# Kernel optimization log

Hardware: AMD Instinct MI355X
Metric: run time of the kernel (lower is better)

## Reference

```python
import jax, jax.numpy as jnp
import numpy as np
from functools import partial

B, S, I, H, O, L = 32, 512, 1024, 1024, 1024, 2


def setup_inputs() -> dict:
    key = jax.random.key(0)
    ks = jax.random.split(key, 7)
    sc = 0.02  # keep gates out of saturation, like nn.Linear init scale
    return {
        "x": jax.random.normal(ks[0], (B, S, I), jnp.float32),
        "h0": jax.random.normal(ks[1], (B, L, H), jnp.float32) * sc,
        "Wx": jax.random.normal(ks[2], (L, 3 * H, I), jnp.float32) * sc,
        "bx": jax.random.normal(ks[3], (L, 3 * H), jnp.float32) * sc,
        "Wh": jax.random.normal(ks[4], (L, 3 * H, H), jnp.float32) * sc,
        "Why": jax.random.normal(ks[5], (O, H), jnp.float32) * sc,
        "bhy": jax.random.normal(ks[6], (O,), jnp.float32) * sc,
    }


def _gru_layer(xproj, h0, Whz, Whr, Whg):
    # xproj: [S, B, 3H] precomputed x-side projections; h0: [B, H]
    def step(h, xp):
        xz, xr, xg = jnp.split(xp, 3, axis=-1)
        z = jax.nn.sigmoid(xz + h @ Whz.T)
        r = jax.nn.sigmoid(xr + h @ Whr.T)
        # NOTE: original code uses sigmoid (not tanh) for the candidate g
        g = jax.nn.sigmoid(xg + (r * h) @ Whg.T)
        h = z * h + (1.0 - z) * g
        return h, h

    hT, ys = jax.lax.scan(step, h0, xproj)
    return hT, ys  # ys: [S, B, H]


def reference(x, h0, Wx, bx, Wh, Why, bhy):
    # x: [B,S,I], h0: [B,L,H]
    inp = x
    finals = []
    for l in range(L):
        # one big GEMM for all timesteps / all three gates on the x side
        xproj = jnp.einsum("bsi,gi->sbg", inp, Wx[l]) + bx[l]  # [S,B,3H]
        Whz, Whr, Whg = jnp.split(Wh[l], 3, axis=0)
        hT, ys = _gru_layer(xproj, h0[:, l, :], Whz, Whr, Whg)
        finals.append(hT)
        inp = jnp.transpose(ys, (1, 0, 2))  # [B,S,H]
    out = jnp.einsum("bsh,oh->bso", inp, Why) + bhy  # [B,S,O]
    hidden = jnp.stack(finals, axis=1)  # [B,L,H]
    return out, hidden
```

## Files before the change

kernel.cpp:

```cpp
#include <hip/hip_runtime.h>
#include <stdint.h>


typedef __bf16 bf16x8 __attribute__((ext_vector_type(8)));
typedef float f32x4 __attribute__((ext_vector_type(4)));
typedef unsigned short u16;
typedef unsigned int u32;
typedef u32 u32x2 __attribute__((ext_vector_type(2)));
typedef u32 u32x4 __attribute__((ext_vector_type(4)));

typedef __attribute__((address_space(1))) u32 as1_u32;
typedef __attribute__((address_space(3))) u32 as3_u32;

__device__ __forceinline__ u16 f2bf(float f) {
  union { float f; u32 u; } a; a.f = f;
  u32 u = a.u;
  u32 r = (u + 0x7fffu + ((u >> 16) & 1u)) >> 16;
  return (u16)r;
}
__device__ __forceinline__ float bf2f(u16 b) {
  union { u32 u; float f; } a; a.u = ((u32)b) << 16;
  return a.f;
}
__device__ __forceinline__ float sigmoidf_(float x) {
  return 1.0f / (1.0f + __expf(-x));
}
__device__ __forceinline__ bf16x8 as_bf(u32x4 q) {
  union { u32x4 q; bf16x8 v; } u; u.q = q; return u.v;
}

#define MFMA16(a, b, c) __builtin_amdgcn_mfma_f32_16x16x32_bf16((a), (b), (c), 0, 0, 0)

__device__ __forceinline__ void gll16(const void* g, void* l) {
  __builtin_amdgcn_global_load_lds((as1_u32*)g, (as3_u32*)l, 16, 0, 0);
}

__device__ __forceinline__ u32x4 ld_sc16(const void* p) {
  u32x4 r;
  asm volatile("global_load_dwordx4 %0, %1, off sc0 sc1" : "=v"(r) : "v"(p) : "memory");
  return r;
}
__device__ __forceinline__ u32x2 ld_sc8(const void* p) {
  u32x2 r;
  asm volatile("global_load_dwordx2 %0, %1, off sc0 sc1" : "=v"(r) : "v"(p) : "memory");
  return r;
}
__device__ __forceinline__ void st_sc2(void* p, u16 v) {
  u32 w = v;
  asm volatile("global_store_short %0, %1, off sc0 sc1" :: "v"(p), "v"(w) : "memory");
}
__device__ __forceinline__ void st_sc8(void* p, u32x2 v) {
  asm volatile("global_store_dwordx2 %0, %1, off sc0 sc1" :: "v"(p), "v"(v) : "memory");
}
__device__ __forceinline__ void st_sc16(void* p, u32x4 v) {
  asm volatile("global_store_dwordx4 %0, %1, off sc0 sc1" :: "v"(p), "v"(v) : "memory");
}
__device__ __forceinline__ void wait_vm0() {
  asm volatile("s_waitcnt vmcnt(0)" ::: "memory");
  __builtin_amdgcn_sched_barrier(0);
}
__device__ __forceinline__ int ldflag(const int* p) {
  int r;
  asm volatile("global_load_dword %0, %1, off sc0 sc1\n\ts_waitcnt vmcnt(0)"
               : "=v"(r) : "v"(p) : "memory");
  return r;
}
__device__ __forceinline__ void stflag(int* p, int v) {
  asm volatile("global_store_dword %0, %1, off sc0 sc1" :: "v"(p), "v"(v) : "memory");
}

__device__ __forceinline__ void signal_flag(int* flag, int val) {
  asm volatile("s_waitcnt vmcnt(0)" ::: "memory");
  __syncthreads();
  if (threadIdx.x == 0) stflag(flag, val);
}
__device__ __forceinline__ void wait_flags(int* flags, int nf, int target, int tid) {
  if (tid < 64) {
    for (;;) {
      int v = (tid < nf) ? ldflag(flags + tid * 32) : target;
      if (__all(v >= target)) break;
      __builtin_amdgcn_s_sleep(2);
    }
  }
  __syncthreads();
}
__device__ __forceinline__ void wait_flags2(int* f1, int n1, int t1,
                                            int* f2, int n2, int t2, int tid) {
  if (tid < 64) {
    const int* addr = nullptr;
    int tgt = 0, active = 0;
    if (tid < n1) { addr = f1 + tid * 32; tgt = t1; active = 1; }
    else if (tid < n1 + n2) { addr = f2 + (tid - n1) * 32; tgt = t2; active = 1; }
    for (;;) {
      int v = active ? ldflag(addr) : 0;
      int sat = (!active) || (v >= tgt);
      if (__all(sat)) break;
      __builtin_amdgcn_s_sleep(2);
    }
  }
  __syncthreads();
}

__device__ __forceinline__ void stage_issue16(const u16* g, u32x4* v, int tid) {
#pragma unroll
  for (int it = 0; it < 4; ++it) {
    int cc = tid + it * 512;
    int row = cc >> 7, sc = cc & 127;
    int gsc = sc ^ (row & 7);
    v[it] = ld_sc16((const char*)g + (size_t)(row * 128 + gsc) * 16);
  }
}
__device__ __forceinline__ void stage_write16(u16* lds, const u32x4* v, int tid) {
#pragma unroll
  for (int it = 0; it < 4; ++it) {
    int cc = tid + it * 512;
    *(u32x4*)((char*)lds + (size_t)cc * 16) = v[it];
  }
}
__device__ __forceinline__ u32x4 read_frag_sw(const u16* lds, int row, int kt, int hi4) {
  int cc = kt * 4 + hi4;
  int sc = cc ^ (row & 7);
  return *(const u32x4*)((const char*)lds + (size_t)row * 2048 + (size_t)sc * 16);
}

__device__ __forceinline__ void load_Bf(u32x4* Bf, const u16* W, int n_g, int hi4) {
  const u16* wrow = W + (size_t)n_g * 1024 + 8 * hi4;
#pragma unroll
  for (int kt = 0; kt < 32; ++kt) Bf[kt] = *(const u32x4*)(wrow + kt * 32);
}

__global__ __launch_bounds__(512, 1) void gru_pipe_kernel(
    const u16* __restrict__ xproj,
    const u16* __restrict__ Whb,
    const u16* __restrict__ Wx1,
    const float* __restrict__ bx,
    const float* __restrict__ h0in,
    u16* __restrict__ h0ring,
    u16* __restrict__ h1_bf,
    u16* __restrict__ rh0,
    u16* __restrict__ rh1,
    float* __restrict__ z0_t,
    float* __restrict__ z1_t,
    u16* __restrict__ xp1t,
    u16* __restrict__ ys1,
    float* __restrict__ hidden,
    int* __restrict__ bar)
{
  __shared__ u16 smem[16 * 1024];
  const int tid = (int)threadIdx.x;
  const int lane = tid & 63;
  const int wv = tid >> 6;
  const int wg = (int)blockIdx.x;
  const int col = lane & 15;
  const int hi4 = lane >> 4;

  int* A0 = bar;
  int* B0 = bar + 1024;
  int* A1 = bar + 1536;
  int* B1 = bar + 2560;
  int* X  = bar + 3072;

  if (wg < 16) {
    const int gw = wg * 8 + wv;
    const int n_g = gw * 16 + col;
    const bool is_z = (wg < 8);
    const int rc = n_g - 1024;
    u32x4 Bf[32];
    load_Bf(Bf, Whb, n_g, hi4);
    for (int s = 0; s < 512; ++s) {
#pragma unroll
      for (int g2 = 0; g2 < 2; ++g2) {
        float xpv[4];
        {
          const u16* xb = xproj + (size_t)s * (32 * 3072) + (size_t)(g2 * 16 + hi4 * 4) * 3072 + n_g;
#pragma unroll
          for (int j = 0; j < 4; ++j) xpv[j] = bf2f(xb[(size_t)j * 3072]);
        }
        wait_flags(B0 + g2 * 256, 8, s, tid);
        u32x4 v[4];
        stage_issue16(h0ring + g2 * 65536 + (size_t)((s - 1) & 3) * 16384, v, tid);
        wait_vm0();
        stage_write16(smem, v, tid);
        __syncthreads();
        f32x4 acc = {0.f, 0.f, 0.f, 0.f};
#pragma unroll
        for (int kt = 0; kt < 32; ++kt)
          acc = MFMA16(as_bf(read_frag_sw(smem, col, kt, hi4)), as_bf(Bf[kt]), acc);
        if (is_z) {
          union { float f[4]; u32x4 q; } q0;
#pragma unroll
          for (int j = 0; j < 4; ++j) q0.f[j] = sigmoidf_(xpv[j] + acc[j]);
          st_sc16(&z0_t[g2 * 16384 + n_g * 16 + hi4 * 4], q0.q);
        } else {
#pragma unroll
          for (int j = 0; j < 4; ++j) {
            int bl = hi4 * 4 + j;
            float rv = sigmoidf_(xpv[j] + acc[j]);
            u16 hraw = smem[bl * 1024 + ((((rc >> 3) ^ (bl & 7)) << 3) | (rc & 7))];
            st_sc2(&rh0[g2 * 16384 + bl * 1024 + rc], f2bf(rv * bf2f(hraw)));
          }
        }
        signal_flag(&A0[g2 * 512 + wg * 32], s + 1);
      }
    }
  } else if (wg < 24) {
    const int wgl = wg - 16;
    const int gw = 128 + wgl * 8 + wv;
    const int n_g = gw * 16 + col;
    const int gc = n_g - 2048;
    u32x4 Bf[32];
    load_Bf(Bf, Whb, n_g, hi4);
    float h_reg[2][4];
#pragma unroll
    for (int g2 = 0; g2 < 2; ++g2)
#pragma unroll
      for (int j = 0; j < 4; ++j)
        h_reg[g2][j] = h0in[(g2 * 16 + hi4 * 4 + j) * 2048 + gc];
    for (int s = 0; s < 512; ++s) {
#pragma unroll
      for (int g2 = 0; g2 < 2; ++g2) {
        float xpv[4];
        {
          const u16* xb = xproj + (size_t)s * (32 * 3072) + (size_t)(g2 * 16 + hi4 * 4) * 3072 + n_g;
#pragma unroll
          for (int j = 0; j < 4; ++j) xpv[j] = bf2f(xb[(size_t)j * 3072]);
        }
        wait_flags2(A0 + g2 * 512, 16, s + 1, X + g2 * 768, 24, s - 3, tid);
        u32x4 v[4];
        stage_issue16(rh0 + g2 * 16384, v, tid);
        u32x4 zq = ld_sc16(&z0_t[g2 * 16384 + gc * 16 + hi4 * 4]);
        wait_vm0();
        stage_write16(smem, v, tid);
        __syncthreads();
        f32x4 acc = {0.f, 0.f, 0.f, 0.f};
#pragma unroll
        for (int kt = 0; kt < 32; ++kt)
          acc = MFMA16(as_bf(read_frag_sw(smem, col, kt, hi4)), as_bf(Bf[kt]), acc);
        union { u32x4 q; float f[4]; } zz; zz.q = zq;
        u16* hslot = h0ring + g2 * 65536 + (size_t)(s & 3) * 16384;
#pragma unroll
        for (int j = 0; j < 4; ++j) {
          int bl = hi4 * 4 + j;
          float gv = sigmoidf_(xpv[j] + acc[j]);
          float hn = zz.f[j] * h_reg[g2][j] + (1.0f - zz.f[j]) * gv;
          h_reg[g2][j] = hn;
          st_sc2(&hslot[bl * 1024 + gc], f2bf(hn));
        }
        signal_flag(&B0[g2 * 256 + wgl * 32], s + 1);
        if (s == 511) {
#pragma unroll
          for (int j = 0; j < 4; ++j)
            hidden[(g2 * 16 + hi4 * 4 + j) * 2048 + gc] = h_reg[g2][j];
        }
      }
    }
  } else if (wg < 48) {
    const int wgx = wg - 24;
    const int gw = wgx * 8 + wv;
    const int n_g = gw * 16 + col;
    u32x4 Bf[32];
    load_Bf(Bf, Wx1, n_g, hi4);
    const float bias = bx[3072 + n_g];
    for (int t = 0; t < 512; ++t) {
#pragma unroll
      for (int g2 = 0; g2 < 2; ++g2) {
        wait_flags2(B0 + g2 * 256, 8, t + 1, B1 + g2 * 256, 8, t - 3, tid);
        u32x4 v[4];
        stage_issue16(h0ring + g2 * 65536 + (size_t)(t & 3) * 16384, v, tid);
        wait_vm0();
        stage_write16(smem, v, tid);
        __syncthreads();
        f32x4 acc = {0.f, 0.f, 0.f, 0.f};
#pragma unroll
        for (int kt = 0; kt < 32; ++kt)
          acc = MFMA16(as_bf(read_frag_sw(smem, col, kt, hi4)), as_bf(Bf[kt]), acc);
        union { u16 o[4]; u32x2 q; } p;
#pragma unroll
        for (int j = 0; j < 4; ++j) p.o[j] = f2bf(acc[j] + bias);
        st_sc8(&xp1t[g2 * 196608 + (size_t)(t & 3) * 49152 + n_g * 16 + hi4 * 4], p.q);
        signal_flag(&X[g2 * 768 + wgx * 32], t + 1);
      }
    }
  } else if (wg < 64) {
    const int wgl = wg - 48;
    const int gw = wgl * 8 + wv;
    const int n_g = gw * 16 + col;
    const bool is_z = (wgl < 8);
    const int rc = n_g - 1024;
    u32x4 Bf[32];
    load_Bf(Bf, Whb + (size_t)3072 * 1024, n_g, hi4);
    for (int s = 0; s < 512; ++s) {
#pragma unroll
      for (int g2 = 0; g2 < 2; ++g2) {
        wait_flags2(X + g2 * 768, 24, s + 1, B1 + g2 * 256, 8, s, tid);
        u32x2 xq = ld_sc8(&xp1t[g2 * 196608 + (size_t)(s & 3) * 49152 + n_g * 16 + hi4 * 4]);
        u32x4 v[4];
        stage_issue16(h1_bf + g2 * 16384, v, tid);
        wait_vm0();
        stage_write16(smem, v, tid);
        __syncthreads();
        float xpv[4];
        {
          union { u32x2 q; u16 o[4]; } xx; xx.q = xq;
#pragma unroll
          for (int j = 0; j < 4; ++j) xpv[j] = bf2f(xx.o[j]);
        }
        f32x4 acc = {0.f, 0.f, 0.f, 0.f};
#pragma unroll
        for (int kt = 0; kt < 32; ++kt)
          acc = MFMA16(as_bf(read_frag_sw(smem, col, kt, hi4)), as_bf(Bf[kt]), acc);
        if (is_z) {
          union { float f[4]; u32x4 q; } q0;
#pragma unroll
          for (int j = 0; j < 4; ++j) q0.f[j] = sigmoidf_(xpv[j] + acc[j]);
          st_sc16(&z1_t[g2 * 16384 + n_g * 16 + hi4 * 4], q0.q);
        } else {
#pragma unroll
          for (int j = 0; j < 4; ++j) {
            int bl = hi4 * 4 + j;
            float rv = sigmoidf_(xpv[j] + acc[j]);
            u16 hraw = smem[bl * 1024 + ((((rc >> 3) ^ (bl & 7)) << 3) | (rc & 7))];
            st_sc2(&rh1[g2 * 16384 + bl * 1024 + rc], f2bf(rv * bf2f(hraw)));
          }
        }
        signal_flag(&A1[g2 * 512 + wgl * 32], s + 1);
      }
    }
  } else {
    const int wgl = wg - 64;
    const int gw = 128 + wgl * 8 + wv;
    const int n_g = gw * 16 + col;
    const int gc = n_g - 2048;
    u32x4 Bf[32];
    load_Bf(Bf, Whb + (size_t)3072 * 1024, n_g, hi4);
    float h_reg[2][4];
#pragma unroll
    for (int g2 = 0; g2 < 2; ++g2)
#pragma unroll
      for (int j = 0; j < 4; ++j)
        h_reg[g2][j] = h0in[(g2 * 16 + hi4 * 4 + j) * 2048 + 1024 + gc];
    for (int s = 0; s < 512; ++s) {
#pragma unroll
      for (int g2 = 0; g2 < 2; ++g2) {
        wait_flags(A1 + g2 * 512, 16, s + 1, tid);
        u32x2 xq = ld_sc8(&xp1t[g2 * 196608 + (size_t)(s & 3) * 49152 + n_g * 16 + hi4 * 4]);
        u32x4 v[4];
        stage_issue16(rh1 + g2 * 16384, v, tid);
        u32x4 zq = ld_sc16(&z1_t[g2 * 16384 + gc * 16 + hi4 * 4]);
        wait_vm0();
        stage_write16(smem, v, tid);
        __syncthreads();
        float xpv[4];
        {
          union { u32x2 q; u16 o[4]; } xx; xx.q = xq;
#pragma unroll
          for (int j = 0; j < 4; ++j) xpv[j] = bf2f(xx.o[j]);
        }
        f32x4 acc = {0.f, 0.f, 0.f, 0.f};
#pragma unroll
        for (int kt = 0; kt < 32; ++kt)
          acc = MFMA16(as_bf(read_frag_sw(smem, col, kt, hi4)), as_bf(Bf[kt]), acc);
        union { u32x4 q; float f[4]; } zz; zz.q = zq;
        u16 hb[4];
#pragma unroll
        for (int j = 0; j < 4; ++j) {
          int bl = hi4 * 4 + j;
          float gv = sigmoidf_(xpv[j] + acc[j]);
          float hn = zz.f[j] * h_reg[g2][j] + (1.0f - zz.f[j]) * gv;
          h_reg[g2][j] = hn;
          hb[j] = f2bf(hn);
          st_sc2(&h1_bf[g2 * 16384 + bl * 1024 + gc], hb[j]);
        }
        signal_flag(&B1[g2 * 256 + wgl * 32], s + 1);
#pragma unroll
        for (int j = 0; j < 4; ++j) {
          int b = g2 * 16 + hi4 * 4 + j;
          ys1[(size_t)b * (512 * 1024) + (size_t)s * 1024 + gc] = hb[j];
        }
        if (s == 511) {
#pragma unroll
          for (int j = 0; j < 4; ++j)
            hidden[(g2 * 16 + hi4 * 4 + j) * 2048 + 1024 + gc] = h_reg[g2][j];
        }
      }
    }
  }
}

template <int MODE>
__global__ __launch_bounds__(256, 1) void gemm_bt_kernel(
    const u16* __restrict__ A, const u16* __restrict__ W,
    const float* __restrict__ bias, void* __restrict__ out,
    int M, int N, int K)
{
  __shared__ u16 At[128 * 32];
  __shared__ u16 Wt[128 * 32];
  const int tid = threadIdx.x;
  const int lane = tid & 63, wv = tid >> 6;
  const int wr = wv >> 1, wc = wv & 1;
  const int m0 = (int)blockIdx.y * 128, n0 = (int)blockIdx.x * 128;
  const int col = lane & 15, hi4 = lane >> 4;
  const size_t K2 = (size_t)K * 2;

  f32x4 acc[4][4];
#pragma unroll
  for (int i = 0; i < 4; ++i)
#pragma unroll
    for (int j = 0; j < 4; ++j) acc[i][j] = (f32x4){0.f, 0.f, 0.f, 0.f};

  const int nkt = K >> 5;
  for (int kt = 0; kt < nkt; ++kt) {
    __syncthreads();
#pragma unroll
    for (int it = 0; it < 2; ++it) {
      int cb = wv * 128 + it * 64;
      int ub = __builtin_amdgcn_readfirstlane(cb);
      int c = cb + lane;
      int row = c >> 2, slot = c & 3;
      int koff = (slot ^ ((row >> 1) & 3)) * 16;
      gll16((const char*)A + (size_t)(m0 + row) * K2 + (size_t)kt * 64 + koff,
            (char*)At + (size_t)ub * 16);
      gll16((const char*)W + (size_t)(n0 + row) * K2 + (size_t)kt * 64 + koff,
            (char*)Wt + (size_t)ub * 16);
    }
    __syncthreads();
    u32x4 Af[4], Wf[4];
#pragma unroll
    for (int i = 0; i < 4; ++i) {
      int row = wr * 64 + i * 16 + col;
      int sc = hi4 ^ ((row >> 1) & 3);
      Af[i] = *(const u32x4*)((const char*)At + (size_t)row * 64 + (size_t)sc * 16);
    }
#pragma unroll
    for (int j = 0; j < 4; ++j) {
      int row = wc * 64 + j * 16 + col;
      int sc = hi4 ^ ((row >> 1) & 3);
      Wf[j] = *(const u32x4*)((const char*)Wt + (size_t)row * 64 + (size_t)sc * 16);
    }
#pragma unroll
    for (int i = 0; i < 4; ++i)
#pragma unroll
      for (int j = 0; j < 4; ++j)
        acc[i][j] = MFMA16(as_bf(Af[i]), as_bf(Wf[j]), acc[i][j]);
  }
#pragma unroll
  for (int i = 0; i < 4; ++i) {
#pragma unroll
    for (int j = 0; j < 4; ++j) {
      int n = n0 + wc * 64 + j * 16 + col;
      float bv = bias[n];
#pragma unroll
      for (int jj = 0; jj < 4; ++jj) {
        int m = m0 + wr * 64 + i * 16 + hi4 * 4 + jj;
        float v = acc[i][j][jj] + bv;
        if (MODE == 0) {
          ((u16*)out)[(size_t)(m & 511) * (32 * 3072) + (size_t)(m >> 9) * 3072 + n] = f2bf(v);
        } else {
          ((float*)out)[(size_t)m * (size_t)N + n] = v;
        }
      }
    }
  }
}

__global__ void cvt_bf_kernel(const float* __restrict__ in, u16* __restrict__ out, int n) {
  int i = ((int)blockIdx.x * 256 + (int)threadIdx.x) * 8;
  if (i + 8 <= n) {
    float4 a = *(const float4*)(in + i);
    float4 b = *(const float4*)(in + i + 4);
    union { u16 o[8]; u32x4 q; } u;
    u.o[0] = f2bf(a.x); u.o[1] = f2bf(a.y); u.o[2] = f2bf(a.z); u.o[3] = f2bf(a.w);
    u.o[4] = f2bf(b.x); u.o[5] = f2bf(b.y); u.o[6] = f2bf(b.z); u.o[7] = f2bf(b.w);
    *(u32x4*)(out + i) = u.q;
  } else {
    for (int k = i; k < n; ++k) out[k] = f2bf(in[k]);
  }
}

__global__ void h0cvt_kernel(const float* __restrict__ h0, u16* __restrict__ h0ring,
                             u16* __restrict__ h1_bf) {
  int i = (int)blockIdx.x * 256 + (int)threadIdx.x;
  if (i < 32768) {
    int b = i >> 10, j = i & 1023;
    int g2 = b >> 4, bl = b & 15;
    h0ring[g2 * 65536 + 3 * 16384 + bl * 1024 + j] = f2bf(h0[b * 2048 + j]);
    h1_bf[g2 * 16384 + bl * 1024 + j] = f2bf(h0[b * 2048 + 1024 + j]);
  }
}

extern "C" void kernel_launch(void* const* d_in, const int* in_sizes, int n_in,
                              void* d_out, int out_size, void* d_ws, size_t ws_size,
                              hipStream_t stream) {
  const float* x   = (const float*)d_in[0];
  const float* h0  = (const float*)d_in[1];
  const float* Wx  = (const float*)d_in[2];
  const float* bx  = (const float*)d_in[3];
  const float* Wh  = (const float*)d_in[4];
  const float* Why = (const float*)d_in[5];
  const float* bhy = (const float*)d_in[6];
  float* out = (float*)d_out;
  float* hidden = out + (size_t)32 * 512 * 1024;

  char* ws = (char*)d_ws;
  u16* xproj  = (u16*)ws;  ws += (size_t)512 * 32 * 3072 * 2;
  u16* ysb    = (u16*)ws;  ws += (size_t)32 * 512 * 1024 * 2;
  u16* xbf    = (u16*)ws;  ws += (size_t)32 * 512 * 1024 * 2;
  u16* Wxb    = (u16*)ws;  ws += (size_t)2 * 3072 * 1024 * 2;
  u16* Whb    = (u16*)ws;  ws += (size_t)2 * 3072 * 1024 * 2;
  u16* Whyb   = (u16*)ws;  ws += (size_t)1024 * 1024 * 2;
  u16* h0ring = (u16*)ws;  ws += 2 * 4 * 16384 * 2;
  u16* h1_bf  = (u16*)ws;  ws += 2 * 16384 * 2;
  u16* rh0    = (u16*)ws;  ws += 2 * 16384 * 2;
  u16* rh1    = (u16*)ws;  ws += 2 * 16384 * 2;
  float* z0_t = (float*)ws; ws += 2 * 16384 * 4;
  float* z1_t = (float*)ws; ws += 2 * 16384 * 4;
  u16* xp1t   = (u16*)ws;  ws += (size_t)2 * 4 * 3072 * 16 * 2;
  int* bar    = (int*)ws;  ws += 32768;

  cvt_bf_kernel<<<(32 * 512 * 1024 / 8 + 255) / 256, 256, 0, stream>>>(x, xbf, 32 * 512 * 1024);
  cvt_bf_kernel<<<(2 * 3072 * 1024 / 8 + 255) / 256, 256, 0, stream>>>(Wx, Wxb, 2 * 3072 * 1024);
  cvt_bf_kernel<<<(2 * 3072 * 1024 / 8 + 255) / 256, 256, 0, stream>>>(Wh, Whb, 2 * 3072 * 1024);
  cvt_bf_kernel<<<(1024 * 1024 / 8 + 255) / 256, 256, 0, stream>>>(Why, Whyb, 1024 * 1024);

  gemm_bt_kernel<0><<<dim3(3072 / 128, 16384 / 128), 256, 0, stream>>>(
      xbf, Wxb, bx, (void*)xproj, 16384, 3072, 1024);
  (void)hipMemsetAsync(bar, 0, 32768, stream);
  h0cvt_kernel<<<128, 256, 0, stream>>>(h0, h0ring, h1_bf);

  gru_pipe_kernel<<<72, 512, 0, stream>>>(
      xproj, Whb, Wxb + (size_t)3072 * 1024, bx, h0,
      h0ring, h1_bf, rh0, rh1, z0_t, z1_t, xp1t, ysb, hidden, bar);

  gemm_bt_kernel<1><<<dim3(1024 / 128, 16384 / 128), 256, 0, stream>>>(
      ysb, Whyb, bhy, (void*)out, 16384, 1024, 1024);
}
```

Baseline: 3.739 ms.

## Speculatively preload next-stage flags during signal and transpose xproj layout

Each signal now also loads the flags the next half-step will wait on, folding that load into the existing vmcnt wait and barrier. The following wait can then skip polling when those values already meet the target. The two batch-half iterations are manually unrolled, and the poll sleep is shortened. The layer-0 xproj layout is transposed to [S][3H][B], so each lane fetches its four batch values with one 8-byte load instead of four strided 2-byte loads.

Result: slower. 4.287 ms (+14.6%).

```diff
diff --git a/kernel.cpp b/kernel.cpp
--- a/kernel.cpp
+++ b/kernel.cpp
@@ -1,5 +1,6 @@
 #include <hip/hip_runtime.h>
 #include <stdint.h>
+#include <limits.h>
 
 
 typedef __bf16 bf16x8 __attribute__((ext_vector_type(8)));
@@ -68,37 +69,53 @@
 __device__ __forceinline__ void stflag(int* p, int v) {
   asm volatile("global_store_dword %0, %1, off sc0 sc1" :: "v"(p), "v"(v) : "memory");
 }
-
-__device__ __forceinline__ void signal_flag(int* flag, int val) {
-  asm volatile("s_waitcnt vmcnt(0)" ::: "memory");
+__device__ __forceinline__ int spec_ld_wait(const int* addr) {
+  int r;
+  asm volatile("global_load_dword %0, %1, off sc0 sc1\n\ts_waitcnt vmcnt(0)"
+               : "=v"(r) : "v"(addr) : "memory");
+  return r;
+}
+
+__device__ __forceinline__ int signal_spec2(int* flag, int val,
+    const int* f1, int n1, const int* f2, int n2, int tid) {
+  int r = 0;
+  if (tid < 64) {
+    const int* addr = f1;
+    if (tid < n1) addr = f1 + tid * 32;
+    else if (tid < n1 + n2) addr = f2 + (tid - n1) * 32;
+    r = spec_ld_wait(addr);
+  } else {
+    asm volatile("s_waitcnt vmcnt(0)" ::: "memory");
+  }
+  __builtin_amdgcn_sched_barrier(0);
   __syncthreads();
   if (threadIdx.x == 0) stflag(flag, val);
-}
-__device__ __forceinline__ void wait_flags(int* flags, int nf, int target, int tid) {
+  return r;
+}
+__device__ __forceinline__ int signal_spec(int* flag, int val,
+    const int* f1, int n1, int tid) {
+  return signal_spec2(flag, val, f1, n1, f1, 0, tid);
+}
+__device__ __forceinline__ void wait_pre2(int* f1, int n1, int t1,
+    int* f2, int n2, int t2, int tid, int spec) {
   if (tid < 64) {
-    for (;;) {
-      int v = (tid < nf) ? ldflag(flags + tid * 32) : target;
-      if (__all(v >= target)) break;
-      __builtin_amdgcn_s_sleep(2);
+    int active = tid < n1 + n2;
+    int tgt = (tid < n1) ? t1 : t2;
+    if (!__all(!active || (spec >= tgt))) {
+      const int* addr = nullptr;
+      if (tid < n1) addr = f1 + tid * 32;
+      else if (tid < n1 + n2) addr = f2 + (tid - n1) * 32;
+      for (;;) {
+        int v = active ? ldflag(addr) : 0x7fffffff;
+        if (__all(!active || (v >= tgt))) break;
+        __builtin_amdgcn_s_sleep(1);
+      }
     }
   }
   __syncthreads();
 }
-__device__ __forceinline__ void wait_flags2(int* f1, int n1, int t1,
-                                            int* f2, int n2, int t2, int tid) {
-  if (tid < 64) {
-    const int* addr = nullptr;
-    int tgt = 0, active = 0;
-    if (tid < n1) { addr = f1 + tid * 32; tgt = t1; active = 1; }
-    else if (tid < n1 + n2) { addr = f2 + (tid - n1) * 32; tgt = t2; active = 1; }
-    for (;;) {
-      int v = active ? ldflag(addr) : 0;
-      int sat = (!active) || (v >= tgt);
-      if (__all(sat)) break;
-      __builtin_amdgcn_s_sleep(2);
-    }
-  }
-  __syncthreads();
+__device__ __forceinline__ void wait_pre(int* f1, int n1, int t1, int tid, int spec) {
+  wait_pre2(f1, n1, t1, f1, 0, 0, tid, spec);
 }
 
 __device__ __forceinline__ void stage_issue16(const u16* g, u32x4* v, int tid) {
@@ -121,6 +138,14 @@
   int cc = kt * 4 + hi4;
   int sc = cc ^ (row & 7);
   return *(const u32x4*)((const char*)lds + (size_t)row * 2048 + (size_t)sc * 16);
+}
+
+__device__ __forceinline__ void load_xpv4(float* xpv, const u16* xproj, int s,
+                                          int n_g, int boff) {
+  union { u32x2 q; u16 o[4]; } xx;
+  xx.q = *(const u32x2*)(xproj + ((size_t)s * 3072 + n_g) * 32 + boff);
+#pragma unroll
+  for (int j = 0; j < 4; ++j) xpv[j] = bf2f(xx.o[j]);
 }
 
 __device__ __forceinline__ void load_Bf(u32x4* Bf, const u16* W, int n_g, int hi4) {
@@ -167,18 +192,14 @@
     const int rc = n_g - 1024;
     u32x4 Bf[32];
     load_Bf(Bf, Whb, n_g, hi4);
+    int specA = INT_MIN, specB = INT_MIN;
     for (int s = 0; s < 512; ++s) {
-#pragma unroll
-      for (int g2 = 0; g2 < 2; ++g2) {
+      {
         float xpv[4];
-        {
-          const u16* xb = xproj + (size_t)s * (32 * 3072) + (size_t)(g2 * 16 + hi4 * 4) * 3072 + n_g;
-#pragma unroll
-          for (int j = 0; j < 4; ++j) xpv[j] = bf2f(xb[(size_t)j * 3072]);
-        }
-        wait_flags(B0 + g2 * 256, 8, s, tid);
-        u32x4 v[4];
-        stage_issue16(h0ring + g2 * 65536 + (size_t)((s - 1) & 3) * 16384, v, tid);
+        load_xpv4(xpv, xproj, s, n_g, hi4 * 4);
+        wait_pre(B0, 8, s, tid, specA);
+        u32x4 v[4];
+        stage_issue16(h0ring + (size_t)((s - 1) & 3) * 16384, v, tid);
         wait_vm0();
         stage_write16(smem, v, tid);
         __syncthreads();
@@ -190,17 +211,46 @@
           union { float f[4]; u32x4 q; } q0;
 #pragma unroll
           for (int j = 0; j < 4; ++j) q0.f[j] = sigmoidf_(xpv[j] + acc[j]);
-          st_sc16(&z0_t[g2 * 16384 + n_g * 16 + hi4 * 4], q0.q);
+          st_sc16(&z0_t[n_g * 16 + hi4 * 4], q0.q);
         } else {
 #pragma unroll
           for (int j = 0; j < 4; ++j) {
             int bl = hi4 * 4 + j;
             float rv = sigmoidf_(xpv[j] + acc[j]);
             u16 hraw = smem[bl * 1024 + ((((rc >> 3) ^ (bl & 7)) << 3) | (rc & 7))];
-            st_sc2(&rh0[g2 * 16384 + bl * 1024 + rc], f2bf(rv * bf2f(hraw)));
+            st_sc2(&rh0[bl * 1024 + rc], f2bf(rv * bf2f(hraw)));
           }
         }
-        signal_flag(&A0[g2 * 512 + wg * 32], s + 1);
+        specB = signal_spec(&A0[wg * 32], s + 1, B0 + 256, 8, tid);
+      }
+      {
+        float xpv[4];
+        load_xpv4(xpv, xproj, s, n_g, 16 + hi4 * 4);
+        wait_pre(B0 + 256, 8, s, tid, specB);
+        u32x4 v[4];
+        stage_issue16(h0ring + 65536 + (size_t)((s - 1) & 3) * 16384, v, tid);
+        wait_vm0();
+        stage_write16(smem, v, tid);
+        __syncthreads();
+        f32x4 acc = {0.f, 0.f, 0.f, 0.f};
+#pragma unroll
+        for (int kt = 0; kt < 32; ++kt)
+          acc = MFMA16(as_bf(read_frag_sw(smem, col, kt, hi4)), as_bf(Bf[kt]), acc);
+        if (is_z) {
+          union { float f[4]; u32x4 q; } q0;
+#pragma unroll
+          for (int j = 0; j < 4; ++j) q0.f[j] = sigmoidf_(xpv[j] + acc[j]);
+          st_sc16(&z0_t[16384 + n_g * 16 + hi4 * 4], q0.q);
+        } else {
+#pragma unroll
+          for (int j = 0; j < 4; ++j) {
+            int bl = hi4 * 4 + j;
+            float rv = sigmoidf_(xpv[j] + acc[j]);
+            u16 hraw = smem[bl * 1024 + ((((rc >> 3) ^ (bl & 7)) << 3) | (rc & 7))];
+            st_sc2(&rh0[16384 + bl * 1024 + rc], f2bf(rv * bf2f(hraw)));
+          }
+        }
+        specA = signal_spec(&A0[512 + wg * 32], s + 1, B0, 8, tid);
       }
     }
   } else if (wg < 24) {
@@ -210,25 +260,21 @@
     const int gc = n_g - 2048;
     u32x4 Bf[32];
     load_Bf(Bf, Whb, n_g, hi4);
-    float h_reg[2][4];
-#pragma unroll
-    for (int g2 = 0; g2 < 2; ++g2)
-#pragma unroll
-      for (int j = 0; j < 4; ++j)
-        h_reg[g2][j] = h0in[(g2 * 16 + hi4 * 4 + j) * 2048 + gc];
+    float hA[4], hB[4];
+#pragma unroll
+    for (int j = 0; j < 4; ++j) {
+      hA[j] = h0in[(hi4 * 4 + j) * 2048 + gc];
+      hB[j] = h0in[(16 + hi4 * 4 + j) * 2048 + gc];
+    }
+    int specA = INT_MIN, specB = INT_MIN;
     for (int s = 0; s < 512; ++s) {
-#pragma unroll
-      for (int g2 = 0; g2 < 2; ++g2) {
+      {
         float xpv[4];
-        {
-          const u16* xb = xproj + (size_t)s * (32 * 3072) + (size_t)(g2 * 16 + hi4 * 4) * 3072 + n_g;
-#pragma unroll
-          for (int j = 0; j < 4; ++j) xpv[j] = bf2f(xb[(size_t)j * 3072]);
-        }
-        wait_flags2(A0 + g2 * 512, 16, s + 1, X + g2 * 768, 24, s - 3, tid);
-        u32x4 v[4];
-        stage_issue16(rh0 + g2 * 16384, v, tid);
-        u32x4 zq = ld_sc16(&z0_t[g2 * 16384 + gc * 16 + hi4 * 4]);
+        load_xpv4(xpv, xproj, s, n_g, hi4 * 4);
+        wait_pre2(A0, 16, s + 1, X, 24, s - 3, tid, specA);
+        u32x4 v[4];
+        stage_issue16(rh0, v, tid);
+        u32x4 zq = ld_sc16(&z0_t[gc * 16 + hi4 * 4]);
         wait_vm0();
         stage_write16(smem, v, tid);
         __syncthreads();
@@ -237,20 +283,49 @@
         for (int kt = 0; kt < 32; ++kt)
           acc = MFMA16(as_bf(read_frag_sw(smem, col, kt, hi4)), as_bf(Bf[kt]), acc);
         union { u32x4 q; float f[4]; } zz; zz.q = zq;
-        u16* hslot = h0ring + g2 * 65536 + (size_t)(s & 3) * 16384;
+        u16* hslot = h0ring + (size_t)(s & 3) * 16384;
 #pragma unroll
         for (int j = 0; j < 4; ++j) {
           int bl = hi4 * 4 + j;
           float gv = sigmoidf_(xpv[j] + acc[j]);
-          float hn = zz.f[j] * h_reg[g2][j] + (1.0f - zz.f[j]) * gv;
-          h_reg[g2][j] = hn;
+          float hn = zz.f[j] * hA[j] + (1.0f - zz.f[j]) * gv;
+          hA[j] = hn;
           st_sc2(&hslot[bl * 1024 + gc], f2bf(hn));
         }
-        signal_flag(&B0[g2 * 256 + wgl * 32], s + 1);
+        specB = signal_spec2(&B0[wgl * 32], s + 1, A0 + 512, 16, X + 768, 24, tid);
         if (s == 511) {
 #pragma unroll
-          for (int j = 0; j < 4; ++j)
-            hidden[(g2 * 16 + hi4 * 4 + j) * 2048 + gc] = h_reg[g2][j];
+          for (int j = 0; j < 4; ++j) hidden[(hi4 * 4 + j) * 2048 + gc] = hA[j];
+        }
+      }
+      {
+        float xpv[4];
+        load_xpv4(xpv, xproj, s, n_g, 16 + hi4 * 4);
+        wait_pre2(A0 + 512, 16, s + 1, X + 768, 24, s - 3, tid, specB);
+        u32x4 v[4];
+        stage_issue16(rh0 + 16384, v, tid);
+        u32x4 zq = ld_sc16(&z0_t[16384 + gc * 16 + hi4 * 4]);
+        wait_vm0();
+        stage_write16(smem, v, tid);
+        __syncthreads();
+        f32x4 acc = {0.f, 0.f, 0.f, 0.f};
+#pragma unroll
+        for (int kt = 0; kt < 32; ++kt)
+          acc = MFMA16(as_bf(read_frag_sw(smem, col, kt, hi4)), as_bf(Bf[kt]), acc);
+        union { u32x4 q; float f[4]; } zz; zz.q = zq;
+        u16* hslot = h0ring + 65536 + (size_t)(s & 3) * 16384;
+#pragma unroll
+        for (int j = 0; j < 4; ++j) {
+          int bl = hi4 * 4 + j;
+          float gv = sigmoidf_(xpv[j] + acc[j]);
+          float hn = zz.f[j] * hB[j] + (1.0f - zz.f[j]) * gv;
+          hB[j] = hn;
+          st_sc2(&hslot[bl * 1024 + gc], f2bf(hn));
+        }
+        specA = signal_spec2(&B0[256 + wgl * 32], s + 1, A0, 16, X, 24, tid);
+        if (s == 511) {
+#pragma unroll
+          for (int j = 0; j < 4; ++j) hidden[(16 + hi4 * 4 + j) * 2048 + gc] = hB[j];
         }
       }
     }
@@ -261,12 +336,12 @@
     u32x4 Bf[32];
     load_Bf(Bf, Wx1, n_g, hi4);
     const float bias = bx[3072 + n_g];
+    int specA = INT_MIN, specB = INT_MIN;
     for (int t = 0; t < 512; ++t) {
-#pragma unroll
-      for (int g2 = 0; g2 < 2; ++g2) {
-        wait_flags2(B0 + g2 * 256, 8, t + 1, B1 + g2 * 256, 8, t - 3, tid);
-        u32x4 v[4];
-        stage_issue16(h0ring + g2 * 65536 + (size_t)(t & 3) * 16384, v, tid);
+      {
+        wait_pre2(B0, 8, t + 1, B1, 8, t - 3, tid, specA);
+        u32x4 v[4];
+        stage_issue16(h0ring + (size_t)(t & 3) * 16384, v, tid);
         wait_vm0();
         stage_write16(smem, v, tid);
         __syncthreads();
@@ -277,8 +352,25 @@
         union { u16 o[4]; u32x2 q; } p;
 #pragma unroll
         for (int j = 0; j < 4; ++j) p.o[j] = f2bf(acc[j] + bias);
-        st_sc8(&xp1t[g2 * 196608 + (size_t)(t & 3) * 49152 + n_g * 16 + hi4 * 4], p.q);
-        signal_flag(&X[g2 * 768 + wgx * 32], t + 1);
+        st_sc8(&xp1t[(size_t)(t & 3) * 49152 + n_g * 16 + hi4 * 4], p.q);
+        specB = signal_spec2(&X[wgx * 32], t + 1, B0 + 256, 8, B1 + 256, 8, tid);
+      }
+      {
+        wait_pre2(B0 + 256, 8, t + 1, B1 + 256, 8, t - 3, tid, specB);
+        u32x4 v[4];
+        stage_issue16(h0ring + 65536 + (size_t)(t & 3) * 16384, v, tid);
+        wait_vm0();
+        stage_write16(smem, v, tid);
+        __syncthreads();
+        f32x4 acc = {0.f, 0.f, 0.f, 0.f};
+#pragma unroll
+        for (int kt = 0; kt < 32; ++kt)
+          acc = MFMA16(as_bf(read_frag_sw(smem, col, kt, hi4)), as_bf(Bf[kt]), acc);
+        union { u16 o[4]; u32x2 q; } p;
+#pragma unroll
+        for (int j = 0; j < 4; ++j) p.o[j] = f2bf(acc[j] + bias);
+        st_sc8(&xp1t[196608 + (size_t)(t & 3) * 49152 + n_g * 16 + hi4 * 4], p.q);
+        specA = signal_spec2(&X[768 + wgx * 32], t + 1, B0, 8, B1, 8, tid);
       }
     }
   } else if (wg < 64) {
@@ -289,13 +381,13 @@
     const int rc = n_g - 1024;
     u32x4 Bf[32];
     load_Bf(Bf, Whb + (size_t)3072 * 1024, n_g, hi4);
+    int specA = INT_MIN, specB = INT_MIN;
     for (int s = 0; s < 512; ++s) {
-#pragma unroll
-      for (int g2 = 0; g2 < 2; ++g2) {
-        wait_flags2(X + g2 * 768, 24, s + 1, B1 + g2 * 256, 8, s, tid);
-        u32x2 xq = ld_sc8(&xp1t[g2 * 196608 + (size_t)(s & 3) * 49152 + n_g * 16 + hi4 * 4]);
-        u32x4 v[4];
-        stage_issue16(h1_bf + g2 * 16384, v, tid);
+      {
+        wait_pre2(X, 24, s + 1, B1, 8, s, tid, specA);
+        u32x2 xq = ld_sc8(&xp1t[(size_t)(s & 3) * 49152 + n_g * 16 + hi4 * 4]);
+        u32x4 v[4];
+        stage_issue16(h1_bf, v, tid);
         wait_vm0();
         stage_write16(smem, v, tid);
         __syncthreads();
@@ -313,17 +405,51 @@
           union { float f[4]; u32x4 q; } q0;
 #pragma unroll
           for (int j = 0; j < 4; ++j) q0.f[j] = sigmoidf_(xpv[j] + acc[j]);
-          st_sc16(&z1_t[g2 * 16384 + n_g * 16 + hi4 * 4], q0.q);
+          st_sc16(&z1_t[n_g * 16 + hi4 * 4], q0.q);
         } else {
 #pragma unroll
           for (int j = 0; j < 4; ++j) {
             int bl = hi4 * 4 + j;
             float rv = sigmoidf_(xpv[j] + acc[j]);
             u16 hraw = smem[bl * 1024 + ((((rc >> 3) ^ (bl & 7)) << 3) | (rc & 7))];
-            st_sc2(&rh1[g2 * 16384 + bl * 1024 + rc], f2bf(rv * bf2f(hraw)));
+            st_sc2(&rh1[bl * 1024 + rc], f2bf(rv * bf2f(hraw)));
           }
         }
-        signal_flag(&A1[g2 * 512 + wgl * 32], s + 1);
+        specB = signal_spec2(&A1[wgl * 32], s + 1, X + 768, 24, B1 + 256, 8, tid);
+      }
+      {
+        wait_pre2(X + 768, 24, s + 1, B1 + 256, 8, s, tid, specB);
+        u32x2 xq = ld_sc8(&xp1t[196608 + (size_t)(s & 3) * 49152 + n_g * 16 + hi4 * 4]);
+        u32x4 v[4];
+        stage_issue16(h1_bf + 16384, v, tid);
+        wait_vm0();
+        stage_write16(smem, v, tid);
+        __syncthreads();
+        float xpv[4];
+        {
+          union { u32x2 q; u16 o[4]; } xx; xx.q = xq;
+#pragma unroll
+          for (int j = 0; j < 4; ++j) xpv[j] = bf2f(xx.o[j]);
+        }
+        f32x4 acc = {0.f, 0.f, 0.f, 0.f};
+#pragma unroll
+        for (int kt = 0; kt < 32; ++kt)
+          acc = MFMA16(as_bf(read_frag_sw(smem, col, kt, hi4)), as_bf(Bf[kt]), acc);
+        if (is_z) {
+          union { float f[4]; u32x4 q; } q0;
+#pragma unroll
+          for (int j = 0; j < 4; ++j) q0.f[j] = sigmoidf_(xpv[j] + acc[j]);
+          st_sc16(&z1_t[16384 + n_g * 16 + hi4 * 4], q0.q);
+        } else {
+#pragma unroll
+          for (int j = 0; j < 4; ++j) {
+            int bl = hi4 * 4 + j;
+            float rv = sigmoidf_(xpv[j] + acc[j]);
+            u16 hraw = smem[bl * 1024 + ((((rc >> 3) ^ (bl & 7)) << 3) | (rc & 7))];
+            st_sc2(&rh1[16384 + bl * 1024 + rc], f2bf(rv * bf2f(hraw)));
+          }
+        }
+        specA = signal_spec2(&A1[512 + wgl * 32], s + 1, X, 24, B1, 8, tid);
       }
     }
   } else {
@@ -333,20 +459,20 @@
     const int gc = n_g - 2048;
     u32x4 Bf[32];
     load_Bf(Bf, Whb + (size_t)3072 * 1024, n_g, hi4);
-    float h_reg[2][4];
-#pragma unroll
-    for (int g2 = 0; g2 < 2; ++g2)
-#pragma unroll
-      for (int j = 0; j < 4; ++j)
-        h_reg[g2][j] = h0in[(g2 * 16 + hi4 * 4 + j) * 2048 + 1024 + gc];
+    float hA[4], hB[4];
+#pragma unroll
+    for (int j = 0; j < 4; ++j) {
+      hA[j] = h0in[(hi4 * 4 + j) * 2048 + 1024 + gc];
+      hB[j] = h0in[(16 + hi4 * 4 + j) * 2048 + 1024 + gc];
+    }
+    int specA = INT_MIN, specB = INT_MIN;
     for (int s = 0; s < 512; ++s) {
-#pragma unroll
-      for (int g2 = 0; g2 < 2; ++g2) {
-        wait_flags(A1 + g2 * 512, 16, s + 1, tid);
-        u32x2 xq = ld_sc8(&xp1t[g2 * 196608 + (size_t)(s & 3) * 49152 + n_g * 16 + hi4 * 4]);
-        u32x4 v[4];
-        stage_issue16(rh1 + g2 * 16384, v, tid);
-        u32x4 zq = ld_sc16(&z1_t[g2 * 16384 + gc * 16 + hi4 * 4]);
+      {
+        wait_pre(A1, 16, s + 1, tid, specA);
+        u32x2 xq = ld_sc8(&xp1t[(size_t)(s & 3) * 49152 + n_g * 16 + hi4 * 4]);
+        u32x4 v[4];
+        stage_issue16(rh1, v, tid);
+        u32x4 zq = ld_sc16(&z1_t[gc * 16 + hi4 * 4]);
         wait_vm0();
         stage_write16(smem, v, tid);
         __syncthreads();
@@ -366,21 +492,61 @@
         for (int j = 0; j < 4; ++j) {
           int bl = hi4 * 4 + j;
           float gv = sigmoidf_(xpv[j] + acc[j]);
-          float hn = zz.f[j] * h_reg[g2][j] + (1.0f - zz.f[j]) * gv;
-          h_reg[g2][j] = hn;
+          float hn = zz.f[j] * hA[j] + (1.0f - zz.f[j]) * gv;
+          hA[j] = hn;
           hb[j] = f2bf(hn);
-          st_sc2(&h1_bf[g2 * 16384 + bl * 1024 + gc], hb[j]);
-        }
-        signal_flag(&B1[g2 * 256 + wgl * 32], s + 1);
+          st_sc2(&h1_bf[bl * 1024 + gc], hb[j]);
+        }
+        specB = signal_spec(&B1[wgl * 32], s + 1, A1 + 512, 16, tid);
 #pragma unroll
         for (int j = 0; j < 4; ++j) {
-          int b = g2 * 16 + hi4 * 4 + j;
+          int b = hi4 * 4 + j;
           ys1[(size_t)b * (512 * 1024) + (size_t)s * 1024 + gc] = hb[j];
         }
         if (s == 511) {
 #pragma unroll
-          for (int j = 0; j < 4; ++j)
-            hidden[(g2 * 16 + hi4 * 4 + j) * 2048 + 1024 + gc] = h_reg[g2][j];
+          for (int j = 0; j < 4; ++j) hidden[(hi4 * 4 + j) * 2048 + 1024 + gc] = hA[j];
+        }
+      }
+      {
+        wait_pre(A1 + 512, 16, s + 1, tid, specB);
+        u32x2 xq = ld_sc8(&xp1t[196608 + (size_t)(s & 3) * 49152 + n_g * 16 + hi4 * 4]);
+        u32x4 v[4];
+        stage_issue16(rh1 + 16384, v, tid);
+        u32x4 zq = ld_sc16(&z1_t[16384 + gc * 16 + hi4 * 4]);
+        wait_vm0();
+        stage_write16(smem, v, tid);
+        __syncthreads();
+        float xpv[4];
+        {
+          union { u32x2 q; u16 o[4]; } xx; xx.q = xq;
+#pragma unroll
+          for (int j = 0; j < 4; ++j) xpv[j] = bf2f(xx.o[j]);
+        }
+        f32x4 acc = {0.f, 0.f, 0.f, 0.f};
+#pragma unroll
+        for (int kt = 0; kt < 32; ++kt)
+          acc = MFMA16(as_bf(read_frag_sw(smem, col, kt, hi4)), as_bf(Bf[kt]), acc);
+        union { u32x4 q; float f[4]; } zz; zz.q = zq;
+        u16 hb[4];
+#pragma unroll
+        for (int j = 0; j < 4; ++j) {
+          int bl = hi4 * 4 + j;
+          float gv = sigmoidf_(xpv[j] + acc[j]);
+          float hn = zz.f[j] * hB[j] + (1.0f - zz.f[j]) * gv;
+          hB[j] = hn;
+          hb[j] = f2bf(hn);
+          st_sc2(&h1_bf[16384 + bl * 1024 + gc], hb[j]);
+        }
+        specA = signal_spec(&B1[256 + wgl * 32], s + 1, A1, 16, tid);
+#pragma unroll
+        for (int j = 0; j < 4; ++j) {
+          int b = 16 + hi4 * 4 + j;
+          ys1[(size_t)b * (512 * 1024) + (size_t)s * 1024 + gc] = hb[j];
+        }
+        if (s == 511) {
+#pragma unroll
+          for (int j = 0; j < 4; ++j) hidden[(16 + hi4 * 4 + j) * 2048 + 1024 + gc] = hB[j];
         }
       }
     }
@@ -454,7 +620,7 @@
         int m = m0 + wr * 64 + i * 16 + hi4 * 4 + jj;
         float v = acc[i][j][jj] + bv;
         if (MODE == 0) {
-          ((u16*)out)[(size_t)(m & 511) * (32 * 3072) + (size_t)(m >> 9) * 3072 + n] = f2bf(v);
+          ((u16*)out)[((size_t)(m & 511) * 3072 + n) * 32 + (m >> 9)] = f2bf(v);
         } else {
           ((float*)out)[(size_t)m * (size_t)N + n] = v;
         }
@@ -502,7 +668,7 @@
   float* hidden = out + (size_t)32 * 512 * 1024;
 
   char* ws = (char*)d_ws;
-  u16* xproj  = (u16*)ws;  ws += (size_t)512 * 32 * 3072 * 2;
+  u16* xproj  = (u16*)ws;  ws += (size_t)512 * 3072 * 32 * 2;
   u16* ysb    = (u16*)ws;  ws += (size_t)32 * 512 * 1024 * 2;
   u16* xbf    = (u16*)ws;  ws += (size_t)32 * 512 * 1024 * 2;
   u16* Wxb    = (u16*)ws;  ws += (size_t)2 * 3072 * 1024 * 2;
```

## Fuse output projection into persistent GRU pipeline as extra workgroup stage

Applied to the files above, without the earlier changes.

Adds 8 workgroups to the persistent GRU kernel that compute the output projection per timestep from a new 4-slot ring of layer-1 hidden states. This replaces the ys1 buffer and the separate final GEMM, overlapping output work with the recurrence. Layer-1 g workgroups now write into the ring and wait on new Y flags so slots are not overwritten before they are consumed. The four conversion kernels are merged into one launch. The risk is added flag traffic and a possible stall in the serial recurrence if the output stage lags.

Result: faster. 3.665 ms (-2.0%).

```diff
diff --git a/kernel.cpp b/kernel.cpp
--- a/kernel.cpp
+++ b/kernel.cpp
@@ -123,6 +123,13 @@
   return *(const u32x4*)((const char*)lds + (size_t)row * 2048 + (size_t)sc * 16);
 }
 
+__device__ __forceinline__ void load_xpv4(float* xpv, const u16* xproj, int s,
+                                          int n_g, int b0) {
+  const u16* xb = xproj + (size_t)s * (32 * 3072) + (size_t)b0 * 3072 + n_g;
+#pragma unroll
+  for (int j = 0; j < 4; ++j) xpv[j] = bf2f(xb[(size_t)j * 3072]);
+}
+
 __device__ __forceinline__ void load_Bf(u32x4* Bf, const u16* W, int n_g, int hi4) {
   const u16* wrow = W + (size_t)n_g * 1024 + 8 * hi4;
 #pragma unroll
@@ -136,13 +143,15 @@
     const float* __restrict__ bx,
     const float* __restrict__ h0in,
     u16* __restrict__ h0ring,
-    u16* __restrict__ h1_bf,
+    u16* __restrict__ h1ring,
     u16* __restrict__ rh0,
     u16* __restrict__ rh1,
     float* __restrict__ z0_t,
     float* __restrict__ z1_t,
     u16* __restrict__ xp1t,
-    u16* __restrict__ ys1,
+    const u16* __restrict__ Why,
+    const float* __restrict__ bhy,
+    float* __restrict__ outp,
     float* __restrict__ hidden,
     int* __restrict__ bar)
 {
@@ -159,6 +168,7 @@
   int* A1 = bar + 1536;
   int* B1 = bar + 2560;
   int* X  = bar + 3072;
+  int* Y  = bar + 4608;
 
   if (wg < 16) {
     const int gw = wg * 8 + wv;
@@ -171,11 +181,7 @@
 #pragma unroll
       for (int g2 = 0; g2 < 2; ++g2) {
         float xpv[4];
-        {
-          const u16* xb = xproj + (size_t)s * (32 * 3072) + (size_t)(g2 * 16 + hi4 * 4) * 3072 + n_g;
-#pragma unroll
-          for (int j = 0; j < 4; ++j) xpv[j] = bf2f(xb[(size_t)j * 3072]);
-        }
+        load_xpv4(xpv, xproj, s, n_g, g2 * 16 + hi4 * 4);
         wait_flags(B0 + g2 * 256, 8, s, tid);
         u32x4 v[4];
         stage_issue16(h0ring + g2 * 65536 + (size_t)((s - 1) & 3) * 16384, v, tid);
@@ -220,11 +226,7 @@
 #pragma unroll
       for (int g2 = 0; g2 < 2; ++g2) {
         float xpv[4];
-        {
-          const u16* xb = xproj + (size_t)s * (32 * 3072) + (size_t)(g2 * 16 + hi4 * 4) * 3072 + n_g;
-#pragma unroll
-          for (int j = 0; j < 4; ++j) xpv[j] = bf2f(xb[(size_t)j * 3072]);
-        }
+        load_xpv4(xpv, xproj, s, n_g, g2 * 16 + hi4 * 4);
         wait_flags2(A0 + g2 * 512, 16, s + 1, X + g2 * 768, 24, s - 3, tid);
         u32x4 v[4];
         stage_issue16(rh0 + g2 * 16384, v, tid);
@@ -295,7 +297,7 @@
         wait_flags2(X + g2 * 768, 24, s + 1, B1 + g2 * 256, 8, s, tid);
         u32x2 xq = ld_sc8(&xp1t[g2 * 196608 + (size_t)(s & 3) * 49152 + n_g * 16 + hi4 * 4]);
         u32x4 v[4];
-        stage_issue16(h1_bf + g2 * 16384, v, tid);
+        stage_issue16(h1ring + g2 * 65536 + (size_t)((s - 1) & 3) * 16384, v, tid);
         wait_vm0();
         stage_write16(smem, v, tid);
         __syncthreads();
@@ -326,7 +328,7 @@
         signal_flag(&A1[g2 * 512 + wgl * 32], s + 1);
       }
     }
-  } else {
+  } else if (wg < 72) {
     const int wgl = wg - 64;
     const int gw = 128 + wgl * 8 + wv;
     const int n_g = gw * 16 + col;
@@ -342,7 +344,7 @@
     for (int s = 0; s < 512; ++s) {
 #pragma unroll
       for (int g2 = 0; g2 < 2; ++g2) {
-        wait_flags(A1 + g2 * 512, 16, s + 1, tid);
+        wait_flags2(A1 + g2 * 512, 16, s + 1, Y + g2 * 256, 8, s - 3, tid);
         u32x2 xq = ld_sc8(&xp1t[g2 * 196608 + (size_t)(s & 3) * 49152 + n_g * 16 + hi4 * 4]);
         u32x4 v[4];
         stage_issue16(rh1 + g2 * 16384, v, tid);
@@ -361,36 +363,57 @@
         for (int kt = 0; kt < 32; ++kt)
           acc = MFMA16(as_bf(read_frag_sw(smem, col, kt, hi4)), as_bf(Bf[kt]), acc);
         union { u32x4 q; float f[4]; } zz; zz.q = zq;
-        u16 hb[4];
+        u16* hslot = h1ring + g2 * 65536 + (size_t)(s & 3) * 16384;
 #pragma unroll
         for (int j = 0; j < 4; ++j) {
           int bl = hi4 * 4 + j;
           float gv = sigmoidf_(xpv[j] + acc[j]);
           float hn = zz.f[j] * h_reg[g2][j] + (1.0f - zz.f[j]) * gv;
           h_reg[g2][j] = hn;
-          hb[j] = f2bf(hn);
-          st_sc2(&h1_bf[g2 * 16384 + bl * 1024 + gc], hb[j]);
+          st_sc2(&hslot[bl * 1024 + gc], f2bf(hn));
         }
         signal_flag(&B1[g2 * 256 + wgl * 32], s + 1);
+        if (s == 511) {
+#pragma unroll
+          for (int j = 0; j < 4; ++j)
+            hidden[(g2 * 16 + hi4 * 4 + j) * 2048 + 1024 + gc] = h_reg[g2][j];
+        }
+      }
+    }
+  } else {
+    const int wgy = wg - 72;
+    const int gw = wgy * 8 + wv;
+    const int n_g = gw * 16 + col;
+    u32x4 Bf[32];
+    load_Bf(Bf, Why, n_g, hi4);
+    const float bias = bhy[n_g];
+    for (int s = 0; s < 512; ++s) {
+#pragma unroll
+      for (int g2 = 0; g2 < 2; ++g2) {
+        wait_flags(B1 + g2 * 256, 8, s + 1, tid);
+        u32x4 v[4];
+        stage_issue16(h1ring + g2 * 65536 + (size_t)(s & 3) * 16384, v, tid);
+        wait_vm0();
+        stage_write16(smem, v, tid);
+        __syncthreads();
+        f32x4 acc = {0.f, 0.f, 0.f, 0.f};
+#pragma unroll
+        for (int kt = 0; kt < 32; ++kt)
+          acc = MFMA16(as_bf(read_frag_sw(smem, col, kt, hi4)), as_bf(Bf[kt]), acc);
 #pragma unroll
         for (int j = 0; j < 4; ++j) {
           int b = g2 * 16 + hi4 * 4 + j;
-          ys1[(size_t)b * (512 * 1024) + (size_t)s * 1024 + gc] = hb[j];
-        }
-        if (s == 511) {
-#pragma unroll
-          for (int j = 0; j < 4; ++j)
-            hidden[(g2 * 16 + hi4 * 4 + j) * 2048 + 1024 + gc] = h_reg[g2][j];
-        }
-      }
-    }
-  }
-}
-
-template <int MODE>
+          outp[(size_t)b * (512 * 1024) + (size_t)s * 1024 + n_g] = acc[j] + bias;
+        }
+        signal_flag(&Y[g2 * 256 + wgy * 32], s + 1);
+      }
+    }
+  }
+}
+
 __global__ __launch_bounds__(256, 1) void gemm_bt_kernel(
     const u16* __restrict__ A, const u16* __restrict__ W,
-    const float* __restrict__ bias, void* __restrict__ out,
+    const float* __restrict__ bias, u16* __restrict__ out,
     int M, int N, int K)
 {
   __shared__ u16 At[128 * 32];
@@ -453,38 +476,39 @@
       for (int jj = 0; jj < 4; ++jj) {
         int m = m0 + wr * 64 + i * 16 + hi4 * 4 + jj;
         float v = acc[i][j][jj] + bv;
-        if (MODE == 0) {
-          ((u16*)out)[(size_t)(m & 511) * (32 * 3072) + (size_t)(m >> 9) * 3072 + n] = f2bf(v);
-        } else {
-          ((float*)out)[(size_t)m * (size_t)N + n] = v;
-        }
-      }
-    }
-  }
-}
-
-__global__ void cvt_bf_kernel(const float* __restrict__ in, u16* __restrict__ out, int n) {
-  int i = ((int)blockIdx.x * 256 + (int)threadIdx.x) * 8;
-  if (i + 8 <= n) {
-    float4 a = *(const float4*)(in + i);
-    float4 b = *(const float4*)(in + i + 4);
-    union { u16 o[8]; u32x4 q; } u;
-    u.o[0] = f2bf(a.x); u.o[1] = f2bf(a.y); u.o[2] = f2bf(a.z); u.o[3] = f2bf(a.w);
-    u.o[4] = f2bf(b.x); u.o[5] = f2bf(b.y); u.o[6] = f2bf(b.z); u.o[7] = f2bf(b.w);
-    *(u32x4*)(out + i) = u.q;
-  } else {
-    for (int k = i; k < n; ++k) out[k] = f2bf(in[k]);
-  }
+        out[(size_t)(m & 511) * (32 * 3072) + (size_t)(m >> 9) * 3072 + n] = f2bf(v);
+      }
+    }
+  }
+}
+
+__global__ void cvt_all_kernel(const float* __restrict__ x, u16* __restrict__ xbf,
+                               const float* __restrict__ Wx, u16* __restrict__ Wxb,
+                               const float* __restrict__ Wh, u16* __restrict__ Whb,
+                               const float* __restrict__ Why, u16* __restrict__ Whyb) {
+  int wg = (int)blockIdx.x;
+  const float* src; u16* dst; int base;
+  if (wg < 8192)       { src = x;   dst = xbf;  base = wg; }
+  else if (wg < 11264) { src = Wx;  dst = Wxb;  base = wg - 8192; }
+  else if (wg < 14336) { src = Wh;  dst = Whb;  base = wg - 11264; }
+  else                 { src = Why; dst = Whyb; base = wg - 14336; }
+  int i = (base * 256 + (int)threadIdx.x) * 8;
+  float4 a = *(const float4*)(src + i);
+  float4 b = *(const float4*)(src + i + 4);
+  union { u16 o[8]; u32x4 q; } u;
+  u.o[0] = f2bf(a.x); u.o[1] = f2bf(a.y); u.o[2] = f2bf(a.z); u.o[3] = f2bf(a.w);
+  u.o[4] = f2bf(b.x); u.o[5] = f2bf(b.y); u.o[6] = f2bf(b.z); u.o[7] = f2bf(b.w);
+  *(u32x4*)(dst + i) = u.q;
 }
 
 __global__ void h0cvt_kernel(const float* __restrict__ h0, u16* __restrict__ h0ring,
-                             u16* __restrict__ h1_bf) {
+                             u16* __restrict__ h1ring) {
   int i = (int)blockIdx.x * 256 + (int)threadIdx.x;
   if (i < 32768) {
     int b = i >> 10, j = i & 1023;
     int g2 = b >> 4, bl = b & 15;
     h0ring[g2 * 65536 + 3 * 16384 + bl * 1024 + j] = f2bf(h0[b * 2048 + j]);
-    h1_bf[g2 * 16384 + bl * 1024 + j] = f2bf(h0[b * 2048 + 1024 + j]);
+    h1ring[g2 * 65536 + 3 * 16384 + bl * 1024 + j] = f2bf(h0[b * 2048 + 1024 + j]);
   }
 }
 
@@ -503,13 +527,12 @@
 
   char* ws = (char*)d_ws;
   u16* xproj  = (u16*)ws;  ws += (size_t)512 * 32 * 3072 * 2;
-  u16* ysb    = (u16*)ws;  ws += (size_t)32 * 512 * 1024 * 2;
   u16* xbf    = (u16*)ws;  ws += (size_t)32 * 512 * 1024 * 2;
   u16* Wxb    = (u16*)ws;  ws += (size_t)2 * 3072 * 1024 * 2;
   u16* Whb    = (u16*)ws;  ws += (size_t)2 * 3072 * 1024 * 2;
   u16* Whyb   = (u16*)ws;  ws += (size_t)1024 * 1024 * 2;
   u16* h0ring = (u16*)ws;  ws += 2 * 4 * 16384 * 2;
-  u16* h1_bf  = (u16*)ws;  ws += 2 * 16384 * 2;
+  u16* h1ring = (u16*)ws;  ws += 2 * 4 * 16384 * 2;
   u16* rh0    = (u16*)ws;  ws += 2 * 16384 * 2;
   u16* rh1    = (u16*)ws;  ws += 2 * 16384 * 2;
   float* z0_t = (float*)ws; ws += 2 * 16384 * 4;
@@ -517,20 +540,15 @@
   u16* xp1t   = (u16*)ws;  ws += (size_t)2 * 4 * 3072 * 16 * 2;
   int* bar    = (int*)ws;  ws += 32768;
 
-  cvt_bf_kernel<<<(32 * 512 * 1024 / 8 + 255) / 256, 256, 0, stream>>>(x, xbf, 32 * 512 * 1024);
-  cvt_bf_kernel<<<(2 * 3072 * 1024 / 8 + 255) / 256, 256, 0, stream>>>(Wx, Wxb, 2 * 3072 * 1024);
-  cvt_bf_kernel<<<(2 * 3072 * 1024 / 8 + 255) / 256, 256, 0, stream>>>(Wh, Whb, 2 * 3072 * 1024);
-  cvt_bf_kernel<<<(1024 * 1024 / 8 + 255) / 256, 256, 0, stream>>>(Why, Whyb, 1024 * 1024);
-
-  gemm_bt_kernel<0><<<dim3(3072 / 128, 16384 / 128), 256, 0, stream>>>(
-      xbf, Wxb, bx, (void*)xproj, 16384, 3072, 1024);
+  cvt_all_kernel<<<14848, 256, 0, stream>>>(x, xbf, Wx, Wxb, Wh, Whb, Why, Whyb);
+
+  gemm_bt_kernel<<<dim3(3072 / 128, 16384 / 128), 256, 0, stream>>>(
+      xbf, Wxb, bx, xproj, 16384, 3072, 1024);
   (void)hipMemsetAsync(bar, 0, 32768, stream);
-  h0cvt_kernel<<<128, 256, 0, stream>>>(h0, h0ring, h1_bf);
-
-  gru_pipe_kernel<<<72, 512, 0, stream>>>(
+  h0cvt_kernel<<<128, 256, 0, stream>>>(h0, h0ring, h1ring);
+
+  gru_pipe_kernel<<<80, 512, 0, stream>>>(
       xproj, Whb, Wxb + (size_t)3072 * 1024, bx, h0,
-      h0ring, h1_bf, rh0, rh1, z0_t, z1_t, xp1t, ysb, hidden, bar);
-
-  gemm_bt_kernel<1><<<dim3(1024 / 128, 16384 / 128), 256, 0, stream>>>(
-      ysb, Whyb, bhy, (void*)out, 16384, 1024, 1024);
-}
+      h0ring, h1ring, rh0, rh1, z0_t, z1_t, xp1t,
+      Whyb, bhy, out, hidden, bar);
+}
```
